# Kernel tuning notes

Measured on AMD Instinct MI355X. Metric: run time of the kernel, lower is better.

The kernel has to match this reference:

```python
import jax, jax.numpy as jnp
import numpy as np

B, C, D = 16, 64, 256          # batch, channels, spatial dim (square input)
K, S, P = 2, 2, 0              # kernel_size, stride, padding
HO = (D + 2 * P - K) // S + 1  # 128


def _build_gather_idx():
    """Precompute the flat pixel indices gathered for each output position.

    Mirrors DeformMaxPool2d.__init__ + the per-(i,j) work in forward():
      1. calculate_index_pool -> top-left corner of each pooling window
      2. new_perm (ImageScrambler on the output grid) scrambles the index map
      3. get_index_pool expands each corner into the KxK window coordinates
      4. retrieve_original_pixels maps each coordinate through perm (pixel-level
         ImageScrambler permutation)
    Result: int array [HO, HO, K*K] of flattened indices into H*W.
    """
    rng = np.random.RandomState(0)
    # 1) window corner indices (calculate_index_pool)
    base = np.arange(-P + K // 2 - 1, D - P + K // 2 - 1, S)  # [HO]
    ci, cj = np.meshgrid(base, base, indexing="ij")           # [HO,HO] each
    centers = np.stack([ci, cj], axis=-1)                     # [HO,HO,2]
    # 2) scramble output-grid positions (new_perm)
    out_perm = rng.permutation(HO * HO)
    centers = centers.reshape(HO * HO, 2)[out_perm].reshape(HO, HO, 2)
    # 3) expand to KxK window coords (get_index_pool ordering: i-major, j-minor)
    offs = np.array([[i, j] for i in range(K) for j in range(K)])  # [K*K,2]
    coords = centers[:, :, None, :] + offs[None, None, :, :]       # [HO,HO,K*K,2]
    flat = coords[..., 0] * D + coords[..., 1]                     # [HO,HO,K*K]
    # 4) map through pixel-level permutation (perm / retrieve_original_pixels)
    pix_perm = rng.permutation(D * D)
    return pix_perm[flat].astype(np.int64)


def setup_inputs() -> dict:
    key = jax.random.key(0)
    x = jax.random.normal(key, (B, C, D, D), dtype=jnp.float32)
    gather_idx = jnp.asarray(_build_gather_idx())  # [HO,HO,K*K] int64
    return {"x": x, "gather_idx": gather_idx}


def reference(x, gather_idx):
    # Fused gather + max: equivalent to the nested (i,j) loops of
    # DeformMaxPool2d.forward, fully vectorized.
    b, c, h, w = x.shape
    x_flat = x.reshape(b, c, h * w)               # [B,C,H*W]
    gathered = x_flat[:, :, gather_idx]           # [B,C,HO,HO,K*K]
    return jnp.max(gathered, axis=-1)             # [B,C,HO,HO]
```

## Files before the change

### kernel.cpp

```cpp
#include <hip/hip_runtime.h>


#define D_DIM     256
#define HO        128
#define PLANE_IN  (D_DIM * D_DIM)
#define PLANE_OUT (HO * HO)
#define NPLANES   (16 * 64)
#define TPB       1024

typedef float          f32x4 __attribute__((ext_vector_type(4)));
typedef unsigned short u16x4 __attribute__((ext_vector_type(4)));

__device__ __forceinline__ unsigned int enc_f32(float f) {
    unsigned int b = __float_as_uint(f);
    return (b & 0x80000000u) ? ~b : (b | 0x80000000u);
}
__device__ __forceinline__ float dec_f32(unsigned int u) {
    unsigned int b = (u & 0x80000000u) ? (u & 0x7FFFFFFFu) : ~u;
    return __uint_as_float(b);
}

__global__ void build_inv_kernel(const int* __restrict__ gidx,
                                 unsigned short* __restrict__ inv) {
    int t = blockIdx.x * blockDim.x + threadIdx.x;
    if (t >= PLANE_OUT) return;
    int4 g = reinterpret_cast<const int4*>(gidx)[t];
    unsigned short o = (unsigned short)t;
    inv[g.x] = o; inv[g.y] = o; inv[g.z] = o; inv[g.w] = o;
}

__launch_bounds__(TPB, 8)
__global__ void pool_scatter_kernel(const float* __restrict__ x,
                                    const unsigned short* __restrict__ inv,
                                    float* __restrict__ out) {
    __shared__ unsigned int so[PLANE_OUT];
    const int tid = threadIdx.x;
    const int bc  = blockIdx.x;

    #pragma unroll
    for (int i = tid; i < PLANE_OUT; i += TPB) so[i] = 0u;
    __syncthreads();

    const f32x4* x4  = reinterpret_cast<const f32x4*>(x + (size_t)bc * PLANE_IN);
    const u16x4* iv4 = reinterpret_cast<const u16x4*>(inv);

    #pragma unroll 4
    for (int i = tid; i < PLANE_IN / 4; i += TPB) {
        f32x4 xv = __builtin_nontemporal_load(&x4[i]);
        u16x4 ov = iv4[i];
        atomicMax(&so[ov.x], enc_f32(xv.x));
        atomicMax(&so[ov.y], enc_f32(xv.y));
        atomicMax(&so[ov.z], enc_f32(xv.z));
        atomicMax(&so[ov.w], enc_f32(xv.w));
    }
    __syncthreads();

    f32x4* out4 = reinterpret_cast<f32x4*>(out + (size_t)bc * PLANE_OUT);
    #pragma unroll
    for (int i = tid; i < PLANE_OUT / 4; i += TPB) {
        unsigned int u0 = so[4 * i + 0], u1 = so[4 * i + 1];
        unsigned int u2 = so[4 * i + 2], u3 = so[4 * i + 3];
        f32x4 r = { dec_f32(u0), dec_f32(u1), dec_f32(u2), dec_f32(u3) };
        __builtin_nontemporal_store(r, &out4[i]);
    }
}

__global__ void pool_gather_kernel(const float* __restrict__ x,
                                   const int* __restrict__ gidx,
                                   float* __restrict__ out) {
    long long t = (long long)blockIdx.x * blockDim.x + threadIdx.x;
    if (t >= (long long)NPLANES * PLANE_OUT) return;
    int pos = (int)(t & (PLANE_OUT - 1));
    int bc  = (int)(t >> 14);
    int4 g = reinterpret_cast<const int4*>(gidx)[pos];
    const float* xp = x + (size_t)bc * PLANE_IN;
    float m = fmaxf(fmaxf(xp[g.x], xp[g.y]), fmaxf(xp[g.z], xp[g.w]));
    out[t] = m;
}

extern "C" void kernel_launch(void* const* d_in, const int* in_sizes, int n_in,
                              void* d_out, int out_size, void* d_ws, size_t ws_size,
                              hipStream_t stream) {
    const float* x    = (const float*)d_in[0];
    const int*   gidx = (const int*)d_in[1];
    float*       out  = (float*)d_out;

    if (ws_size >= (size_t)PLANE_IN * sizeof(unsigned short)) {
        unsigned short* inv = (unsigned short*)d_ws;
        build_inv_kernel<<<PLANE_OUT / 256, 256, 0, stream>>>(gidx, inv);
        pool_scatter_kernel<<<NPLANES, TPB, 0, stream>>>(x, inv, out);
    } else {
        long long total = (long long)NPLANES * PLANE_OUT;
        pool_gather_kernel<<<(int)((total + 255) / 256), 256, 0, stream>>>(x, gidx, out);
    }
}
```

Before: 353.9 us.

## Replace inverse-index LDS atomic scatter with chunked shared-memory gather per plane

Removes the inverse-index build kernel and the LDS atomicMax scatter. Each block now streams its input plane into shared memory in four 64KB chunks. After each chunk, every thread checks its 16 output positions' four gather indices against the chunk range and folds in the matching values with max. This avoids atomics and the encode/decode step. In exchange, each thread rereads the gather index array once per chunk, adds extra syncs, and does range checks whose branches may diverge.

```diff
diff --git a/kernel.cpp b/kernel.cpp
--- a/kernel.cpp
+++ b/kernel.cpp
@@ -7,75 +7,57 @@
 #define PLANE_OUT (HO * HO)
 #define NPLANES   (16 * 64)
 #define TPB       1024
+#define CHUNK     16384
+#define NCHUNK    (PLANE_IN / CHUNK)
+#define OPT       (PLANE_OUT / TPB)
 
-typedef float          f32x4 __attribute__((ext_vector_type(4)));
-typedef unsigned short u16x4 __attribute__((ext_vector_type(4)));
-
-__device__ __forceinline__ unsigned int enc_f32(float f) {
-    unsigned int b = __float_as_uint(f);
-    return (b & 0x80000000u) ? ~b : (b | 0x80000000u);
-}
-__device__ __forceinline__ float dec_f32(unsigned int u) {
-    unsigned int b = (u & 0x80000000u) ? (u & 0x7FFFFFFFu) : ~u;
-    return __uint_as_float(b);
-}
-
-__global__ void build_inv_kernel(const int* __restrict__ gidx,
-                                 unsigned short* __restrict__ inv) {
-    int t = blockIdx.x * blockDim.x + threadIdx.x;
-    if (t >= PLANE_OUT) return;
-    int4 g = reinterpret_cast<const int4*>(gidx)[t];
-    unsigned short o = (unsigned short)t;
-    inv[g.x] = o; inv[g.y] = o; inv[g.z] = o; inv[g.w] = o;
-}
+typedef float f32x4 __attribute__((ext_vector_type(4)));
 
 __launch_bounds__(TPB, 8)
-__global__ void pool_scatter_kernel(const float* __restrict__ x,
-                                    const unsigned short* __restrict__ inv,
-                                    float* __restrict__ out) {
-    __shared__ unsigned int so[PLANE_OUT];
+__global__ void pool_chunk_gather(const float* __restrict__ x,
+                                  const int* __restrict__ gidx,
+                                  float* __restrict__ out) {
+    __shared__ float sx[CHUNK];
     const int tid = threadIdx.x;
     const int bc  = blockIdx.x;
 
+    const f32x4* xp4 = reinterpret_cast<const f32x4*>(x + (size_t)bc * PLANE_IN);
+    const int4*  g4  = reinterpret_cast<const int4*>(gidx);
+
+    float acc[OPT];
     #pragma unroll
-    for (int i = tid; i < PLANE_OUT; i += TPB) so[i] = 0u;
-    __syncthreads();
+    for (int k = 0; k < OPT; ++k) acc[k] = -__builtin_inff();
 
-    const f32x4* x4  = reinterpret_cast<const f32x4*>(x + (size_t)bc * PLANE_IN);
-    const u16x4* iv4 = reinterpret_cast<const u16x4*>(inv);
+    for (int c = 0; c < NCHUNK; ++c) {
+        __syncthreads();
+        f32x4* s4 = reinterpret_cast<f32x4*>(sx);
+        #pragma unroll
+        for (int i = 0; i < CHUNK / 4 / TPB; ++i) {
+            s4[i * TPB + tid] =
+                __builtin_nontemporal_load(&xp4[c * (CHUNK / 4) + i * TPB + tid]);
+        }
+        __syncthreads();
 
-    #pragma unroll 4
-    for (int i = tid; i < PLANE_IN / 4; i += TPB) {
-        f32x4 xv = __builtin_nontemporal_load(&x4[i]);
-        u16x4 ov = iv4[i];
-        atomicMax(&so[ov.x], enc_f32(xv.x));
-        atomicMax(&so[ov.y], enc_f32(xv.y));
-        atomicMax(&so[ov.z], enc_f32(xv.z));
-        atomicMax(&so[ov.w], enc_f32(xv.w));
+        const unsigned lo = (unsigned)(c * CHUNK);
+        #pragma unroll 4
+        for (int k = 0; k < OPT; ++k) {
+            int4 g = g4[k * TPB + tid];
+            unsigned dx = (unsigned)g.x - lo;
+            unsigned dy = (unsigned)g.y - lo;
+            unsigned dz = (unsigned)g.z - lo;
+            unsigned dw = (unsigned)g.w - lo;
+            if (dx < (unsigned)CHUNK) acc[k] = fmaxf(acc[k], sx[dx]);
+            if (dy < (unsigned)CHUNK) acc[k] = fmaxf(acc[k], sx[dy]);
+            if (dz < (unsigned)CHUNK) acc[k] = fmaxf(acc[k], sx[dz]);
+            if (dw < (unsigned)CHUNK) acc[k] = fmaxf(acc[k], sx[dw]);
+        }
     }
-    __syncthreads();
 
-    f32x4* out4 = reinterpret_cast<f32x4*>(out + (size_t)bc * PLANE_OUT);
+    float* op = out + (size_t)bc * PLANE_OUT;
     #pragma unroll
-    for (int i = tid; i < PLANE_OUT / 4; i += TPB) {
-        unsigned int u0 = so[4 * i + 0], u1 = so[4 * i + 1];
-        unsigned int u2 = so[4 * i + 2], u3 = so[4 * i + 3];
-        f32x4 r = { dec_f32(u0), dec_f32(u1), dec_f32(u2), dec_f32(u3) };
-        __builtin_nontemporal_store(r, &out4[i]);
+    for (int k = 0; k < OPT; ++k) {
+        __builtin_nontemporal_store(acc[k], &op[k * TPB + tid]);
     }
-}
-
-__global__ void pool_gather_kernel(const float* __restrict__ x,
-                                   const int* __restrict__ gidx,
-                                   float* __restrict__ out) {
-    long long t = (long long)blockIdx.x * blockDim.x + threadIdx.x;
-    if (t >= (long long)NPLANES * PLANE_OUT) return;
-    int pos = (int)(t & (PLANE_OUT - 1));
-    int bc  = (int)(t >> 14);
-    int4 g = reinterpret_cast<const int4*>(gidx)[pos];
-    const float* xp = x + (size_t)bc * PLANE_IN;
-    float m = fmaxf(fmaxf(xp[g.x], xp[g.y]), fmaxf(xp[g.z], xp[g.w]));
-    out[t] = m;
 }
 
 extern "C" void kernel_launch(void* const* d_in, const int* in_sizes, int n_in,
@@ -84,13 +66,6 @@
     const float* x    = (const float*)d_in[0];
     const int*   gidx = (const int*)d_in[1];
     float*       out  = (float*)d_out;
-
-    if (ws_size >= (size_t)PLANE_IN * sizeof(unsigned short)) {
-        unsigned short* inv = (unsigned short*)d_ws;
-        build_inv_kernel<<<PLANE_OUT / 256, 256, 0, stream>>>(gidx, inv);
-        pool_scatter_kernel<<<NPLANES, TPB, 0, stream>>>(x, inv, out);
-    } else {
-        long long total = (long long)NPLANES * PLANE_OUT;
-        pool_gather_kernel<<<(int)((total + 255) / 256), 256, 0, stream>>>(x, gidx, out);
-    }
+    (void)d_ws; (void)ws_size;
+    pool_chunk_gather<<<NPLANES, TPB, 0, stream>>>(x, gidx, out);
 }
```

Result: slower. 412.0 us (+16.4%).
